# Performance work log

Measured on AMD Instinct MI355X. Metric: run time of the kernel, lower is better.

The kernel has to match this reference:

```python
import jax, jax.numpy as jnp
import numpy as np

N_NODES = 100000
N_EDGES = 1000000
N_QUERY = 100000
F_IN = 64
HIDDEN = 64
LABEL_DIM = 2


def setup_inputs() -> dict:
    key = jax.random.key(0)
    ks = jax.random.split(key, 16)
    inp = {}
    for i, nm in enumerate(["Xr", "Xi", "Xj", "Xk"]):
        inp[nm] = jax.random.normal(ks[i], (N_NODES, F_IN), dtype=jnp.float32)
    for i, nm in enumerate(["norm_r", "norm_i", "norm_j", "norm_k"]):
        inp[nm] = jax.random.normal(ks[4 + i], (N_EDGES,), dtype=jnp.float32) * 0.1
    inp["edge_index"] = jax.random.randint(ks[8], (2, N_EDGES), 0, N_NODES)
    inp["query_edges"] = jax.random.randint(ks[9], (N_QUERY, 2), 0, N_NODES)
    s1 = (2.0 / (F_IN + HIDDEN)) ** 0.5  # glorot
    inp["W1"] = jax.random.normal(ks[10], (4, F_IN, HIDDEN), dtype=jnp.float32) * s1
    inp["b1"] = jnp.zeros((4, HIDDEN), dtype=jnp.float32)
    s2 = (2.0 / (HIDDEN + HIDDEN)) ** 0.5
    inp["W2"] = jax.random.normal(ks[11], (4, HIDDEN, HIDDEN), dtype=jnp.float32) * s2
    inp["b2"] = jnp.zeros((4, HIDDEN), dtype=jnp.float32)
    inp["Cw"] = jax.random.normal(ks[12], (LABEL_DIM, 8 * HIDDEN), dtype=jnp.float32) * 0.05
    inp["Cb"] = jnp.zeros((LABEL_DIM,), dtype=jnp.float32)
    return inp


def _quaconv(Xs, src, dst, norms, W, b, n_nodes):
    # Xs: list of 4 [N,F] components; norms: list of 4 [E] Laplacian norms.
    # P[a][b] = propagate(X_a, -norm_b) = scatter_add over dst of (-norm_b)_e * X_a[src_e]
    P = []
    for a in range(4):
        G = Xs[a][src]  # [E, F] gather, reused for all 4 norms
        P.append([jax.ops.segment_sum((-norms[b])[:, None] * G, dst, num_segments=n_nodes)
                  for b in range(4)])
    Tr = P[0][0] - P[1][1] - P[2][2] - P[3][3]
    Ti = P[1][0] + P[0][1] + P[3][2] - P[2][3]
    Tj = P[2][0] - P[3][1] + P[0][2] + P[1][3]
    Tk = P[3][0] + P[2][1] - P[1][2] + P[0][3]
    Wr, Wi, Wj, Wk = W[0], W[1], W[2], W[3]
    out_r = Tr @ Wr - Ti @ Wi - Tj @ Wj - Tk @ Wk + b[0]
    out_i = Tr @ Wi + Ti @ Wr + Tj @ Wk - Tk @ Wj + b[1]
    out_j = Tr @ Wj - Ti @ Wk + Tj @ Wr + Tk @ Wi + b[2]
    out_k = Tr @ Wk + Ti @ Wj - Tj @ Wi + Tk @ Wr + b[3]
    return out_r, out_i, out_j, out_k


def _forward(Xr, Xi, Xj, Xk, norm_r, norm_i, norm_j, norm_k,
             W1, b1, W2, b2, Cw, Cb, edge_index, query_edges):
    src, dst = edge_index[0], edge_index[1]
    n = Xr.shape[0]
    norms = [norm_r, norm_i, norm_j, norm_k]
    Xs = [Xr, Xi, Xj, Xk]
    for W, b in ((W1, b1), (W2, b2)):
        Xs = list(_quaconv(Xs, src, dst, norms, W, b, n))
        # complex_relu_layer_different: mask = 1.0*(x>=0); mask*x == relu(x)
        Xs = [jax.nn.relu(x) for x in Xs]
    q0, q1 = query_edges[:, 0], query_edges[:, 1]
    # cat(real[q0], real[q1], imag_i[q0], imag_i[q1], ...) -> [Eq, 8*hidden]
    feats = jnp.concatenate([c[idx] for c in Xs for idx in (q0, q1)], axis=-1)
    # dropout is identity at inference; Conv1d(kernel=1) == linear over channels
    logits = feats @ Cw.T + Cb  # [Eq, label_dim]
    return jax.nn.log_softmax(logits, axis=-1)


def reference(Xr, Xi, Xj, Xk, norm_r, norm_i, norm_j, norm_k,
              W1, b1, W2, b2, Cw, Cb, edge_index, query_edges):
    return _forward(Xr, Xi, Xj, Xk, norm_r, norm_i, norm_j, norm_k,
                    W1, b1, W2, b2, Cw, Cb, edge_index, query_edges)
```

## Files before the change

kernel.cpp:

```cpp
#include <hip/hip_runtime.h>
#include <hip/hip_bf16.h>

#define N_NODESC 100000
#define N_EDGESC 1000000
#define N_QUERYC 100000

typedef short short8 __attribute__((ext_vector_type(8)));
typedef short s16x2 __attribute__((ext_vector_type(2)));
typedef float f32x4 __attribute__((ext_vector_type(4)));

__device__ __forceinline__ float ldf(const void* p, int i, int isbf) {
  return isbf ? __bfloat162float(((const __hip_bfloat16*)p)[i])
              : ((const float*)p)[i];
}
__device__ __forceinline__ unsigned short f2b(float x) {
  __hip_bfloat16 h = __float2bfloat16(x);
  return *(unsigned short*)&h;
}
__device__ __forceinline__ float b2f(unsigned int u) {
  return __uint_as_float(u << 16);
}
__device__ __forceinline__ s16x2 u2s(unsigned u) {
  union { unsigned u; s16x2 s; } c; c.u = u; return c.s;
}
__device__ __forceinline__ void gload16(const void* g, void* l) {
  __builtin_amdgcn_global_load_lds(
      (const __attribute__((address_space(1))) void*)g,
      (__attribute__((address_space(3))) void*)l, 16, 0, 0);
}

__global__ void k_sniff(const void* x, int* flag) {
  __shared__ int cnt;
  int t = threadIdx.x;
  if (t == 0) cnt = 0;
  __syncthreads();
  const unsigned short* h = (const unsigned short*)x;
  int local = 0;
  for (int i = t; i < 4096; i += 256) {
    int e = (h[i] >> 7) & 0xFF;
    if (e >= 107 && e <= 133) local++;
  }
  atomicAdd(&cnt, local);
  __syncthreads();
  if (t == 0) *flag = (cnt >= 3482) ? 1 : 0;
}

__global__ void k_hist(const int* __restrict__ dst, int* __restrict__ cnt, int ne) {
  int e = blockIdx.x * 256 + threadIdx.x;
  if (e < ne) atomicAdd(&cnt[dst[e]], 1);
}

__global__ void k_scan1(const int* __restrict__ cnt, int* __restrict__ off,
                        int* __restrict__ partials, int n) {
  __shared__ int s[1024];
  int t = threadIdx.x;
  int idx = blockIdx.x * 1024 + t;
  int v = (idx < n) ? cnt[idx] : 0;
  s[t] = v;
  __syncthreads();
  for (int d = 1; d < 1024; d <<= 1) {
    int tmp = (t >= d) ? s[t - d] : 0;
    __syncthreads();
    s[t] += tmp;
    __syncthreads();
  }
  if (idx < n) off[idx] = s[t] - v;
  if (t == 1023) partials[blockIdx.x] = s[1023];
}

__global__ void k_scan2(const int* __restrict__ partials, int* __restrict__ pref,
                        int* __restrict__ off, int nb, int npos) {
  __shared__ int s[128];
  int t = threadIdx.x;
  int v = (t < nb) ? partials[t] : 0;
  s[t] = v;
  __syncthreads();
  for (int d = 1; d < 128; d <<= 1) {
    int tmp = (t >= d) ? s[t - d] : 0;
    __syncthreads();
    s[t] += tmp;
    __syncthreads();
  }
  if (t < nb) pref[t] = s[t] - v;
  if (t == 127) off[npos] = s[127];
}

__global__ void k_scan3(int* __restrict__ off, const int* __restrict__ pref,
                        int* __restrict__ cursor, int n) {
  int i = blockIdx.x * 256 + threadIdx.x;
  if (i < n) {
    int o = off[i] + pref[i >> 10];
    off[i] = o;
    cursor[i] = o;
  }
}

__global__ void k_fill(const int* __restrict__ ei,
                       const void* nr, const void* ni, const void* nj, const void* nk,
                       const int* __restrict__ flagp, int* __restrict__ cursor,
                       uint4* __restrict__ recs, int ne) {
  int isbf = *flagp;
  int e = blockIdx.x * 256 + threadIdx.x;
  if (e >= ne) return;
  int s = ei[e];
  int d = ei[ne + e];
  int pos = atomicAdd(&cursor[d], 1);
  uint4 r;
  r.x = (unsigned)s;
  r.y = (unsigned)f2b(-ldf(nr, e, isbf)) | ((unsigned)f2b(-ldf(ni, e, isbf)) << 16);
  r.z = (unsigned)f2b(-ldf(nj, e, isbf)) | ((unsigned)f2b(-ldf(nk, e, isbf)) << 16);
  r.w = 0;
  recs[pos] = r;
}

__global__ __launch_bounds__(256) void k_ilv(
    const void* X0, const void* X1, const void* X2, const void* X3,
    const int* __restrict__ flagp, unsigned short* __restrict__ Xg, int n) {
  int isbf = *flagp;
  int lane = threadIdx.x & 63;
  int node = blockIdx.x * 4 + (threadIdx.x >> 6);
  if (node >= n) return;
  int idx = node * 64 + lane;
  unsigned int lo = f2b(ldf(X0, idx, isbf)) | ((unsigned int)f2b(ldf(X1, idx, isbf)) << 16);
  unsigned int hi = f2b(ldf(X2, idx, isbf)) | ((unsigned int)f2b(ldf(X3, idx, isbf)) << 16);
  uint2 g = make_uint2(lo, hi);
  *(uint2*)(Xg + (size_t)node * 256 + lane * 4) = g;
}

#if __has_builtin(__builtin_amdgcn_fdot2_f32_bf16)
#define USE_DOT2 1
#else
#define USE_DOT2 0
#endif
__global__ __launch_bounds__(128, 8) void k_agg(
    const unsigned short* __restrict__ Xg, const int* __restrict__ off,
    const uint4* __restrict__ recs, unsigned short* __restrict__ Tf, int nnodes) {
  __shared__ unsigned short tl4[2][4][256];
  int lane = threadIdx.x & 63;
  int w = threadIdx.x >> 6;
  int gq = blockIdx.x * 2 + w;
  int n0 = gq * 4;
  if (n0 >= nnodes) return;

  int o_[5];
#pragma unroll
  for (int i = 0; i < 5; i++) o_[i] = __builtin_amdgcn_readfirstlane(off[n0 + i]);

#pragma unroll
  for (int n = 0; n < 4; ++n) {
    int rs = o_[n], re = o_[n + 1];
    float tr = 0.f, ti = 0.f, tj = 0.f, tk = 0.f;

    auto qacc = [&](uint2 g, unsigned mx, unsigned my) {
#if USE_DOT2
      unsigned a = mx, b = my;
      unsigned sa = (a >> 16) | (a << 16);
      unsigned sb = (b >> 16) | (b << 16);
      unsigned A1 = a ^ 0x80000000u;
      unsigned A2 = b ^ 0x80008000u;
      unsigned B2 = sb ^ 0x00008000u;
      unsigned D2 = sb ^ 0x80000000u;
      s16x2 gx = u2s(g.x), gy = u2s(g.y);
      tr = __builtin_amdgcn_fdot2_f32_bf16(u2s(A1), gx, tr, false);
      tr = __builtin_amdgcn_fdot2_f32_bf16(u2s(A2), gy, tr, false);
      ti = __builtin_amdgcn_fdot2_f32_bf16(u2s(sa), gx, ti, false);
      ti = __builtin_amdgcn_fdot2_f32_bf16(u2s(B2), gy, ti, false);
      tj = __builtin_amdgcn_fdot2_f32_bf16(u2s(b),  gx, tj, false);
      tj = __builtin_amdgcn_fdot2_f32_bf16(u2s(A1), gy, tj, false);
      tk = __builtin_amdgcn_fdot2_f32_bf16(u2s(D2), gx, tk, false);
      tk = __builtin_amdgcn_fdot2_f32_bf16(u2s(sa), gy, tk, false);
#else
      float mr = __uint_as_float(mx << 16), mi = __uint_as_float(mx & 0xffff0000u);
      float mj = __uint_as_float(my << 16), mk = __uint_as_float(my & 0xffff0000u);
      float xr = __uint_as_float(g.x << 16), xi = __uint_as_float(g.x & 0xffff0000u);
      float xj = __uint_as_float(g.y << 16), xk = __uint_as_float(g.y & 0xffff0000u);
      tr += mr * xr - mi * xi - mj * xj - mk * xk;
      ti += mr * xi + mi * xr + mj * xk - mk * xj;
      tj += mr * xj - mi * xk + mj * xr + mk * xi;
      tk += mr * xk + mi * xj - mj * xi + mk * xr;
#endif
    };

    int e = rs;
    for (; e + 8 <= re; e += 8) {
      uint4 r[8];
#pragma unroll
      for (int u = 0; u < 8; u++) r[u] = recs[e + u];
      int ss[8];
      unsigned sx[8], sy[8];
#pragma unroll
      for (int u = 0; u < 8; u++) {
        ss[u] = __builtin_amdgcn_readfirstlane((int)r[u].x);
        sx[u] = __builtin_amdgcn_readfirstlane(r[u].y);
        sy[u] = __builtin_amdgcn_readfirstlane(r[u].z);
      }
      uint2 g[8];
#pragma unroll
      for (int u = 0; u < 8; u++)
        g[u] = *(const uint2*)(Xg + (size_t)ss[u] * 256 + lane * 4);
#pragma unroll
      for (int u = 0; u < 8; u++) qacc(g[u], sx[u], sy[u]);
    }
    for (; e < re; ++e) {
      uint4 r = recs[e];
      int s = __builtin_amdgcn_readfirstlane((int)r.x);
      unsigned mx = __builtin_amdgcn_readfirstlane(r.y);
      unsigned my = __builtin_amdgcn_readfirstlane(r.z);
      uint2 g0 = *(const uint2*)(Xg + (size_t)s * 256 + lane * 4);
      qacc(g0, mx, my);
    }

    tl4[w][n][lane] = f2b(tr);
    tl4[w][n][64 + lane] = f2b(ti);
    tl4[w][n][128 + lane] = f2b(tj);
    tl4[w][n][192 + lane] = f2b(tk);
  }
  __builtin_amdgcn_wave_barrier();

  size_t blk = (size_t)(gq >> 2) * 4096;
  int qi = gq & 3;
#pragma unroll
  for (int h = 0; h < 2; ++h) {
    int m = h * 64 + lane;
    int n = m & 3, l = m >> 2;
    uint4 v = *(const uint4*)&tl4[w][n][l * 8];
    size_t o = blk + (size_t)(l >> 2) * 512 + (l & 3) * 128 + qi * 32 + n * 8;
    *(uint4*)(Tf + o) = v;
  }
}

__global__ void k_weff(const void* W, const void* b, const int* __restrict__ flagp,
                       unsigned short* __restrict__ Wq, float* __restrict__ bcat) {
  int isbf = *flagp;
  int t = blockIdx.x * 256 + threadIdx.x;
  int w4 = t >> 12;
  int h = (t >> 6) & 63;
  int kk = t & 63;
  int s = (kk >> 3) ^ (h & 7);
  Wq[(w4 * 64 + h) * 64 + s * 8 + (kk & 7)] = f2b(ldf(W, w4 * 4096 + kk * 64 + h, isbf));
  if (t < 256) bcat[t] = ldf(b, t, isbf);
}

__global__ __launch_bounds__(256, 2) void k_gemm(
    const unsigned short* __restrict__ A, const unsigned short* __restrict__ Wq,
    const float* __restrict__ bias, int M, int mode,
    unsigned short* __restrict__ XgOut,
    float* __restrict__ P, const void* Cw, const int* __restrict__ flagp) {
  __shared__ unsigned short Wsm[16384];

  int t = threadIdx.x;
  int lane = t & 63;
  int w = t >> 6;
  int l15 = lane & 15, quad = lane >> 4;
  int m0 = blockIdx.x * 64;
  int hh = (w & 1) * 32;

#pragma unroll
  for (int i = 0; i < 8; i++)
    gload16((const char*)Wq + (size_t)(i * 256 + t) * 16,
            (char*)Wsm + (size_t)(i * 256 + w * 64) * 16);
  __syncthreads();

  short8 av[2][8];
  int n16 = blockIdx.x * 4 + (w >> 1) * 2;
#pragma unroll
  for (int mi = 0; mi < 2; mi++)
#pragma unroll
    for (int kc = 0; kc < 8; kc++)
      av[mi][kc] = *(const short8*)(A + (size_t)(n16 + mi) * 4096 + kc * 512 + lane * 8);

  f32x4 acc[2][4][2];
#pragma unroll
  for (int mi = 0; mi < 2; mi++)
#pragma unroll
    for (int c = 0; c < 4; c++)
#pragma unroll
      for (int hb = 0; hb < 2; hb++) acc[mi][c][hb] = (f32x4){0.f, 0.f, 0.f, 0.f};

#pragma unroll
  for (int kc = 0; kc < 8; kc++) {
    int a = kc >> 1;
    short8 bv[4][2];
#pragma unroll
    for (int c = 0; c < 4; c++) {
      int w4 = a ^ c;
      int neg = (0x3950 >> (a * 4 + c)) & 1;
#pragma unroll
      for (int hb = 0; hb < 2; hb++) {
        int h = hh + hb * 16 + l15;
        int lc = ((kc & 1) * 4 + quad) ^ (l15 & 7);
        short8 bb = *(const short8*)&Wsm[(w4 * 64 + h) * 64 + lc * 8];
        if (neg) {
          uint4 u = *(uint4*)&bb;
          u.x ^= 0x80008000u; u.y ^= 0x80008000u;
          u.z ^= 0x80008000u; u.w ^= 0x80008000u;
          bb = *(short8*)&u;
        }
        bv[c][hb] = bb;
      }
    }
#pragma unroll
    for (int mi = 0; mi < 2; mi++)
#pragma unroll
      for (int c = 0; c < 4; c++)
#pragma unroll
        for (int hb = 0; hb < 2; hb++)
          acc[mi][c][hb] =
              __builtin_amdgcn_mfma_f32_16x16x32_bf16(av[mi][kc], bv[c][hb], acc[mi][c][hb], 0, 0, 0);
  }

  float bias_v[4][2];
#pragma unroll
  for (int c = 0; c < 4; c++)
#pragma unroll
    for (int hb = 0; hb < 2; hb++) bias_v[c][hb] = bias[c * 64 + hh + hb * 16 + l15];

  if (mode == 0) {
#pragma unroll
    for (int mi = 0; mi < 2; mi++) {
#pragma unroll
      for (int hb = 0; hb < 2; hb++) {
#pragma unroll
        for (int r = 0; r < 4; r++) {
          int node = m0 + (w >> 1) * 32 + mi * 16 + quad * 4 + r;
          unsigned int lo =
              f2b(fmaxf(acc[mi][0][hb][r] + bias_v[0][hb], 0.f)) |
              ((unsigned int)f2b(fmaxf(acc[mi][1][hb][r] + bias_v[1][hb], 0.f)) << 16);
          unsigned int hi =
              f2b(fmaxf(acc[mi][2][hb][r] + bias_v[2][hb], 0.f)) |
              ((unsigned int)f2b(fmaxf(acc[mi][3][hb][r] + bias_v[3][hb], 0.f)) << 16);
          *(uint2*)(XgOut + (size_t)node * 256 + (hh + hb * 16 + l15) * 4) =
              make_uint2(lo, hi);
        }
      }
    }
  } else {
    int isbf = *flagp;
    float cw[4][2][4];
#pragma unroll
    for (int c = 0; c < 4; c++)
#pragma unroll
      for (int hb = 0; hb < 2; hb++) {
        int h = hh + hb * 16 + l15;
#pragma unroll
        for (int d = 0; d < 2; d++)
#pragma unroll
          for (int e = 0; e < 2; e++)
            cw[c][hb][e + 2 * d] = ldf(Cw, d * 512 + c * 128 + e * 64 + h, isbf);
      }
#pragma unroll
    for (int mi = 0; mi < 2; mi++) {
#pragma unroll
      for (int r = 0; r < 4; r++) {
        int node = m0 + (w >> 1) * 32 + mi * 16 + quad * 4 + r;
        float pd0 = 0.f, pd1 = 0.f, pd2 = 0.f, pd3 = 0.f;
#pragma unroll
        for (int c = 0; c < 4; c++)
#pragma unroll
          for (int hb = 0; hb < 2; hb++) {
            float v = fmaxf(acc[mi][c][hb][r] + bias_v[c][hb], 0.f);
            pd0 += v * cw[c][hb][0];
            pd1 += v * cw[c][hb][1];
            pd2 += v * cw[c][hb][2];
            pd3 += v * cw[c][hb][3];
          }
#pragma unroll
        for (int o = 1; o < 16; o <<= 1) {
          pd0 += __shfl_xor(pd0, o);
          pd1 += __shfl_xor(pd1, o);
          pd2 += __shfl_xor(pd2, o);
          pd3 += __shfl_xor(pd3, o);
        }
        if (l15 == 0 && node < M) {
          atomicAdd(&P[node * 4 + 0], pd0);
          atomicAdd(&P[node * 4 + 1], pd1);
          atomicAdd(&P[node * 4 + 2], pd2);
          atomicAdd(&P[node * 4 + 3], pd3);
        }
      }
    }
  }
}

__global__ void k_query(const int* __restrict__ qe, const float* __restrict__ P,
                        const void* Cb, const int* __restrict__ flagp,
                        void* out, int nq) {
  int isbf = *flagp;
  int q = blockIdx.x * 256 + threadIdx.x;
  if (q >= nq) return;
  int q0 = qe[q * 2], q1 = qe[q * 2 + 1];
  float l0 = P[q0 * 4 + 0] + P[q1 * 4 + 1] + ldf(Cb, 0, isbf);
  float l1 = P[q0 * 4 + 2] + P[q1 * 4 + 3] + ldf(Cb, 1, isbf);
  float m = fmaxf(l0, l1);
  float lse = m + logf(expf(l0 - m) + expf(l1 - m));
  float o0 = l0 - lse, o1 = l1 - lse;
  if (isbf) {
    __hip_bfloat16* o = (__hip_bfloat16*)out;
    o[q * 2] = __float2bfloat16(o0);
    o[q * 2 + 1] = __float2bfloat16(o1);
  } else {
    float* o = (float*)out;
    o[q * 2] = o0;
    o[q * 2 + 1] = o1;
  }
}

extern "C" void kernel_launch(void* const* d_in, const int* in_sizes, int n_in,
                              void* d_out, int out_size, void* d_ws, size_t ws_size,
                              hipStream_t stream) {
  const int N = N_NODESC, NE = N_EDGESC, NQ = N_QUERYC;
  const int NPAD = 100224;

  char* w = (char*)d_ws;
  auto alloc = [&](size_t bytes) -> void* {
    void* p = (void*)w;
    w += (bytes + 255) & ~(size_t)255;
    return p;
  };
  int* flag       = (int*)alloc(4);
  int* offsets    = (int*)alloc((size_t)(N + 1) * 4);
  int* cursor     = (int*)alloc((size_t)N * 4);
  int* partials   = (int*)alloc(128 * 4);
  int* pref       = (int*)alloc(128 * 4);
  uint4* recs     = (uint4*)alloc((size_t)NE * 16);
  unsigned short* Tf = (unsigned short*)alloc((size_t)NPAD * 256 * 2);
  unsigned short* Xg = (unsigned short*)alloc((size_t)NPAD * 256 * 2);
  unsigned short* Wq = (unsigned short*)alloc(16384 * 2);
  float* bcat     = (float*)alloc(256 * 4);
  float* P        = (float*)alloc((size_t)N * 4 * 4);
  (void)ws_size; (void)n_in; (void)in_sizes; (void)out_size;

  const int* ei = (const int*)d_in[8];

  k_sniff<<<1, 256, 0, stream>>>(d_in[0], flag);

  hipMemsetAsync(cursor, 0, (size_t)N * 4, stream);
  hipMemsetAsync(P, 0, (size_t)N * 16, stream);
  k_hist<<<(NE + 255) / 256, 256, 0, stream>>>(ei + NE, cursor, NE);
  k_scan1<<<(N + 1023) / 1024, 1024, 0, stream>>>(cursor, offsets, partials, N);
  k_scan2<<<1, 128, 0, stream>>>(partials, pref, offsets, (N + 1023) / 1024, N);
  k_scan3<<<(N + 255) / 256, 256, 0, stream>>>(offsets, pref, cursor, N);
  k_fill<<<(NE + 255) / 256, 256, 0, stream>>>(ei, d_in[4], d_in[5], d_in[6], d_in[7],
                                               flag, cursor, recs, NE);

  k_ilv<<<(N + 3) / 4, 256, 0, stream>>>(d_in[0], d_in[1], d_in[2], d_in[3], flag, Xg, N);

  int ggrid = (N + 63) / 64;
  int nquads = (N + 3) / 4;
  int agrid = (nquads + 1) / 2;

  k_agg<<<agrid, 128, 0, stream>>>(Xg, offsets, recs, Tf, N);
  k_weff<<<64, 256, 0, stream>>>(d_in[10], d_in[11], flag, Wq, bcat);
  k_gemm<<<ggrid, 256, 0, stream>>>(Tf, Wq, bcat, N, 0, Xg, nullptr, nullptr, flag);

  k_agg<<<agrid, 128, 0, stream>>>(Xg, offsets, recs, Tf, N);
  k_weff<<<64, 256, 0, stream>>>(d_in[12], d_in[13], flag, Wq, bcat);
  k_gemm<<<ggrid, 256, 0, stream>>>(Tf, Wq, bcat, N, 1, nullptr, P, d_in[14], flag);

  k_query<<<(NQ + 255) / 256, 256, 0, stream>>>((const int*)d_in[9], P, d_in[15],
                                                flag, d_out, NQ);
}
```

Baseline: 552.6 us.

## Merge prep kernels, drop memsets, and replace P atomics with split stores

Folds the format sniff and cursor zeroing into one kernel and replaces both memsets. The histogram and input interleave now run as two block ranges of a single launch, and both weight-prep launches become one. The classifier epilogue writes per-half partial logits to two buffers with plain vector stores instead of float atomics, which also removes the need to zero P. The query kernel sums the two halves. The aim is to cut launch count and atomic traffic, at the cost of one more small buffer and more reads in the query kernel.

```diff
diff --git a/kernel.cpp b/kernel.cpp
--- a/kernel.cpp
+++ b/kernel.cpp
@@ -29,25 +29,47 @@
       (__attribute__((address_space(3))) void*)l, 16, 0, 0);
 }
 
-__global__ void k_sniff(const void* x, int* flag) {
-  __shared__ int cnt;
+__global__ void k_prep(const void* x, int* flag, int* cnt, int n) {
+  int bid = blockIdx.x;
   int t = threadIdx.x;
-  if (t == 0) cnt = 0;
-  __syncthreads();
-  const unsigned short* h = (const unsigned short*)x;
-  int local = 0;
-  for (int i = t; i < 4096; i += 256) {
-    int e = (h[i] >> 7) & 0xFF;
-    if (e >= 107 && e <= 133) local++;
-  }
-  atomicAdd(&cnt, local);
-  __syncthreads();
-  if (t == 0) *flag = (cnt >= 3482) ? 1 : 0;
-}
-
-__global__ void k_hist(const int* __restrict__ dst, int* __restrict__ cnt, int ne) {
-  int e = blockIdx.x * 256 + threadIdx.x;
-  if (e < ne) atomicAdd(&cnt[dst[e]], 1);
+  if (bid == 0) {
+    __shared__ int scnt;
+    if (t == 0) scnt = 0;
+    __syncthreads();
+    const unsigned short* h = (const unsigned short*)x;
+    int local = 0;
+    for (int i = t; i < 4096; i += 256) {
+      int e = (h[i] >> 7) & 0xFF;
+      if (e >= 107 && e <= 133) local++;
+    }
+    atomicAdd(&scnt, local);
+    __syncthreads();
+    if (t == 0) *flag = (scnt >= 3482) ? 1 : 0;
+  } else {
+    int i = (bid - 1) * 256 + t;
+    if (i < n) cnt[i] = 0;
+  }
+}
+
+__global__ __launch_bounds__(256) void k_hist_ilv(
+    const int* __restrict__ ei, int* __restrict__ cnt, int ne, int histBlocks,
+    const void* X0, const void* X1, const void* X2, const void* X3,
+    const int* __restrict__ flagp, unsigned short* __restrict__ Xg, int n) {
+  int bid = blockIdx.x;
+  if (bid < histBlocks) {
+    int e = bid * 256 + threadIdx.x;
+    if (e < ne) atomicAdd(&cnt[ei[ne + e]], 1);
+  } else {
+    int isbf = *flagp;
+    int lane = threadIdx.x & 63;
+    int node = (bid - histBlocks) * 4 + (threadIdx.x >> 6);
+    if (node >= n) return;
+    int idx = node * 64 + lane;
+    unsigned int lo = f2b(ldf(X0, idx, isbf)) | ((unsigned int)f2b(ldf(X1, idx, isbf)) << 16);
+    unsigned int hi = f2b(ldf(X2, idx, isbf)) | ((unsigned int)f2b(ldf(X3, idx, isbf)) << 16);
+    uint2 g = make_uint2(lo, hi);
+    *(uint2*)(Xg + (size_t)node * 256 + lane * 4) = g;
+  }
 }
 
 __global__ void k_scan1(const int* __restrict__ cnt, int* __restrict__ off,
@@ -111,20 +133,6 @@
   r.z = (unsigned)f2b(-ldf(nj, e, isbf)) | ((unsigned)f2b(-ldf(nk, e, isbf)) << 16);
   r.w = 0;
   recs[pos] = r;
-}
-
-__global__ __launch_bounds__(256) void k_ilv(
-    const void* X0, const void* X1, const void* X2, const void* X3,
-    const int* __restrict__ flagp, unsigned short* __restrict__ Xg, int n) {
-  int isbf = *flagp;
-  int lane = threadIdx.x & 63;
-  int node = blockIdx.x * 4 + (threadIdx.x >> 6);
-  if (node >= n) return;
-  int idx = node * 64 + lane;
-  unsigned int lo = f2b(ldf(X0, idx, isbf)) | ((unsigned int)f2b(ldf(X1, idx, isbf)) << 16);
-  unsigned int hi = f2b(ldf(X2, idx, isbf)) | ((unsigned int)f2b(ldf(X3, idx, isbf)) << 16);
-  uint2 g = make_uint2(lo, hi);
-  *(uint2*)(Xg + (size_t)node * 256 + lane * 4) = g;
 }
 
 #if __has_builtin(__builtin_amdgcn_fdot2_f32_bf16)
@@ -229,10 +237,17 @@
   }
 }
 
-__global__ void k_weff(const void* W, const void* b, const int* __restrict__ flagp,
-                       unsigned short* __restrict__ Wq, float* __restrict__ bcat) {
+__global__ void k_weff2(const void* W1, const void* b1, const void* W2, const void* b2,
+                        const int* __restrict__ flagp,
+                        unsigned short* __restrict__ Wq1, float* __restrict__ bcat1,
+                        unsigned short* __restrict__ Wq2, float* __restrict__ bcat2) {
   int isbf = *flagp;
-  int t = blockIdx.x * 256 + threadIdx.x;
+  int layer = blockIdx.x >> 6;
+  const void* W = layer ? W2 : W1;
+  const void* b = layer ? b2 : b1;
+  unsigned short* Wq = layer ? Wq2 : Wq1;
+  float* bcat = layer ? bcat2 : bcat1;
+  int t = (blockIdx.x & 63) * 256 + threadIdx.x;
   int w4 = t >> 12;
   int h = (t >> 6) & 63;
   int kk = t & 63;
@@ -245,7 +260,8 @@
     const unsigned short* __restrict__ A, const unsigned short* __restrict__ Wq,
     const float* __restrict__ bias, int M, int mode,
     unsigned short* __restrict__ XgOut,
-    float* __restrict__ P, const void* Cw, const int* __restrict__ flagp) {
+    float* __restrict__ P1, float* __restrict__ P2,
+    const void* Cw, const int* __restrict__ flagp) {
   __shared__ unsigned short Wsm[16384];
 
   int t = threadIdx.x;
@@ -348,6 +364,7 @@
           for (int e = 0; e < 2; e++)
             cw[c][hb][e + 2 * d] = ldf(Cw, d * 512 + c * 128 + e * 64 + h, isbf);
       }
+    float* Pout = (hh == 0) ? P1 : P2;
 #pragma unroll
     for (int mi = 0; mi < 2; mi++) {
 #pragma unroll
@@ -372,25 +389,28 @@
           pd3 += __shfl_xor(pd3, o);
         }
         if (l15 == 0 && node < M) {
-          atomicAdd(&P[node * 4 + 0], pd0);
-          atomicAdd(&P[node * 4 + 1], pd1);
-          atomicAdd(&P[node * 4 + 2], pd2);
-          atomicAdd(&P[node * 4 + 3], pd3);
+          f32x4 st = {pd0, pd1, pd2, pd3};
+          *(f32x4*)(Pout + (size_t)node * 4) = st;
         }
       }
     }
   }
 }
 
-__global__ void k_query(const int* __restrict__ qe, const float* __restrict__ P,
+__global__ void k_query(const int* __restrict__ qe,
+                        const float* __restrict__ P1, const float* __restrict__ P2,
                         const void* Cb, const int* __restrict__ flagp,
                         void* out, int nq) {
   int isbf = *flagp;
   int q = blockIdx.x * 256 + threadIdx.x;
   if (q >= nq) return;
   int q0 = qe[q * 2], q1 = qe[q * 2 + 1];
-  float l0 = P[q0 * 4 + 0] + P[q1 * 4 + 1] + ldf(Cb, 0, isbf);
-  float l1 = P[q0 * 4 + 2] + P[q1 * 4 + 3] + ldf(Cb, 1, isbf);
+  f32x4 a0 = *(const f32x4*)(P1 + (size_t)q0 * 4);
+  f32x4 b0 = *(const f32x4*)(P2 + (size_t)q0 * 4);
+  f32x4 a1 = *(const f32x4*)(P1 + (size_t)q1 * 4);
+  f32x4 b1 = *(const f32x4*)(P2 + (size_t)q1 * 4);
+  float l0 = (a0[0] + b0[0]) + (a1[1] + b1[1]) + ldf(Cb, 0, isbf);
+  float l1 = (a0[2] + b0[2]) + (a1[3] + b1[3]) + ldf(Cb, 1, isbf);
   float m = fmaxf(l0, l1);
   float lse = m + logf(expf(l0 - m) + expf(l1 - m));
   float o0 = l0 - lse, o1 = l1 - lse;
@@ -425,38 +445,45 @@
   uint4* recs     = (uint4*)alloc((size_t)NE * 16);
   unsigned short* Tf = (unsigned short*)alloc((size_t)NPAD * 256 * 2);
   unsigned short* Xg = (unsigned short*)alloc((size_t)NPAD * 256 * 2);
-  unsigned short* Wq = (unsigned short*)alloc(16384 * 2);
-  float* bcat     = (float*)alloc(256 * 4);
-  float* P        = (float*)alloc((size_t)N * 4 * 4);
+  unsigned short* Wq1 = (unsigned short*)alloc(16384 * 2);
+  unsigned short* Wq2 = (unsigned short*)alloc(16384 * 2);
+  float* bcat1    = (float*)alloc(256 * 4);
+  float* bcat2    = (float*)alloc(256 * 4);
+  float* P1       = (float*)alloc((size_t)N * 4 * 4);
+  float* P2       = (float*)alloc((size_t)N * 4 * 4);
   (void)ws_size; (void)n_in; (void)in_sizes; (void)out_size;
 
   const int* ei = (const int*)d_in[8];
 
-  k_sniff<<<1, 256, 0, stream>>>(d_in[0], flag);
-
-  hipMemsetAsync(cursor, 0, (size_t)N * 4, stream);
-  hipMemsetAsync(P, 0, (size_t)N * 16, stream);
-  k_hist<<<(NE + 255) / 256, 256, 0, stream>>>(ei + NE, cursor, NE);
+  k_prep<<<392, 256, 0, stream>>>(d_in[0], flag, cursor, N);
+
+  k_weff2<<<128, 256, 0, stream>>>(d_in[10], d_in[11], d_in[12], d_in[13], flag,
+                                   Wq1, bcat1, Wq2, bcat2);
+
+  int histBlocks = (NE + 255) / 256;
+  int ilvBlocks = (N + 3) / 4;
+  k_hist_ilv<<<histBlocks + ilvBlocks, 256, 0, stream>>>(
+      ei, cursor, NE, histBlocks,
+      d_in[0], d_in[1], d_in[2], d_in[3], flag, Xg, N);
+
   k_scan1<<<(N + 1023) / 1024, 1024, 0, stream>>>(cursor, offsets, partials, N);
   k_scan2<<<1, 128, 0, stream>>>(partials, pref, offsets, (N + 1023) / 1024, N);
   k_scan3<<<(N + 255) / 256, 256, 0, stream>>>(offsets, pref, cursor, N);
   k_fill<<<(NE + 255) / 256, 256, 0, stream>>>(ei, d_in[4], d_in[5], d_in[6], d_in[7],
                                                flag, cursor, recs, NE);
 
-  k_ilv<<<(N + 3) / 4, 256, 0, stream>>>(d_in[0], d_in[1], d_in[2], d_in[3], flag, Xg, N);
-
   int ggrid = (N + 63) / 64;
   int nquads = (N + 3) / 4;
   int agrid = (nquads + 1) / 2;
 
   k_agg<<<agrid, 128, 0, stream>>>(Xg, offsets, recs, Tf, N);
-  k_weff<<<64, 256, 0, stream>>>(d_in[10], d_in[11], flag, Wq, bcat);
-  k_gemm<<<ggrid, 256, 0, stream>>>(Tf, Wq, bcat, N, 0, Xg, nullptr, nullptr, flag);
+  k_gemm<<<ggrid, 256, 0, stream>>>(Tf, Wq1, bcat1, N, 0, Xg, nullptr, nullptr,
+                                    nullptr, flag);
 
   k_agg<<<agrid, 128, 0, stream>>>(Xg, offsets, recs, Tf, N);
-  k_weff<<<64, 256, 0, stream>>>(d_in[12], d_in[13], flag, Wq, bcat);
-  k_gemm<<<ggrid, 256, 0, stream>>>(Tf, Wq, bcat, N, 1, nullptr, P, d_in[14], flag);
-
-  k_query<<<(NQ + 255) / 256, 256, 0, stream>>>((const int*)d_in[9], P, d_in[15],
-                                                flag, d_out, NQ);
-}
+  k_gemm<<<ggrid, 256, 0, stream>>>(Tf, Wq2, bcat2, N, 1, nullptr, P1, P2,
+                                    d_in[14], flag);
+
+  k_query<<<(NQ + 255) / 256, 256, 0, stream>>>((const int*)d_in[9], P1, P2,
+                                                d_in[15], flag, d_out, NQ);
+}
```

Result: faster. 509.1 us (-7.9%).
